# Performance work log

Hardware: AMD Instinct MI355X
Metric: run time of the kernel (lower is better)

The kernel has to match this reference:

```python
import jax, jax.numpy as jnp
import numpy as np

BS = 512          # number of nodes (batch)
EMBED = 256       # embed_dim
NHEAD = 8
HDIM = EMBED // NHEAD
E = BS * BS       # fully-connected intra-batch graph


def _xavier(key, shape):
    lim = float(np.sqrt(6.0 / (shape[0] + shape[1])))
    return jax.random.uniform(key, shape, jnp.float32, -lim, lim)


def setup_inputs() -> dict:
    key = jax.random.key(0)
    ks = jax.random.split(key, 6)
    feats = jax.random.normal(ks[0], (BS, EMBED), jnp.float32)
    # edges sorted by destination c, exactly BS edges per destination
    dst = jnp.repeat(jnp.arange(BS), BS)   # c
    src = jnp.tile(jnp.arange(BS), BS)     # r
    edge_index = jnp.stack([src, dst], axis=1).astype(jnp.int32)  # [E, 2], cols (r, c)
    edge_attr = jnp.zeros((E, 1), jnp.float32)  # unused by forward
    return {
        "feats": feats,
        "edge_index": edge_index,
        "edge_attr": edge_attr,
        "Wq": _xavier(ks[1], (EMBED, EMBED)), "bq": jnp.zeros((EMBED,), jnp.float32),
        "Wk": _xavier(ks[2], (EMBED, EMBED)), "bk": jnp.zeros((EMBED,), jnp.float32),
        "Wv": _xavier(ks[3], (EMBED, EMBED)), "bv": jnp.zeros((EMBED,), jnp.float32),
        "Wo": _xavier(ks[4], (EMBED, EMBED)), "bo": jnp.zeros((EMBED,), jnp.float32),
    }


def reference(feats, edge_index, edge_attr, Wq, bq, Wk, bk, Wv, bv, Wo, bo):
    bs = feats.shape[0]
    scale = 1.0 / np.sqrt(HDIM)
    # QKV projections (torch Linear: x @ W.T + b), split heads -> [h, n, d]
    q = (feats @ Wq.T + bq).reshape(bs, NHEAD, HDIM).transpose(1, 0, 2)
    k = (feats @ Wk.T + bk).reshape(bs, NHEAD, HDIM).transpose(1, 0, 2)
    v = (feats @ Wv.T + bv).reshape(bs, NHEAD, HDIM).transpose(1, 0, 2)
    r, c = edge_index[:, 0], edge_index[:, 1]
    qe = q[:, c, :]   # [h, E, d] query of destination node
    ke = k[:, r, :]   # [h, E, d] key of source node
    ve = v[:, r, :]   # [h, E, d] value of source node
    sim = jnp.einsum('hed,hed->eh', qe, ke) * scale   # [E, h]
    # deterministic segment softmax over edges grouped by destination c
    m = jax.ops.segment_max(sim, c, num_segments=bs)  # [n, h]
    p = jnp.exp(sim - m[c])
    s = jax.ops.segment_sum(p, c, num_segments=bs)    # [n, h]
    attn = p / s[c]                                    # [E, h]
    # weight values and scatter-add per destination (aggr='add')
    out_e = attn.T[..., None] * ve                     # [h, E, d]
    out_e = out_e.transpose(1, 0, 2).reshape(-1, NHEAD * HDIM)  # [E, h*d]
    agg = jax.ops.segment_sum(out_e, c, num_segments=bs)        # [n, embed]
    return agg @ Wo.T + bo
```

## Files before the change

kernel.cpp:

```cpp
#include <hip/hip_runtime.h>

#define BS 512
#define EMBED 256
#define NHEAD 8
#define HDIM 32

typedef __attribute__((ext_vector_type(8))) short short8;
typedef __attribute__((ext_vector_type(4))) float f32x4;

__device__ inline f32x4 mfma16(short8 a, short8 b, f32x4 c) {
    return __builtin_amdgcn_mfma_f32_16x16x32_bf16(a, b, c, 0, 0, 0);
}

__device__ inline unsigned short f2bf(float x) {
    unsigned int u = __float_as_uint(x);
    u += 0x7FFFu + ((u >> 16) & 1u);
    return (unsigned short)(u >> 16);
}
__device__ inline short8 cvt8(const float* p) {
    float4 a = *(const float4*)p;
    float4 b = *(const float4*)(p + 4);
    float x[8] = {a.x, a.y, a.z, a.w, b.x, b.y, b.z, b.w};
    short8 hi;
#pragma unroll
    for (int j = 0; j < 8; ++j) hi[j] = (short)f2bf(x[j]);
    return hi;
}

__global__ __launch_bounds__(256) void qkv_fused(
    const float* __restrict__ feats,
    const float* __restrict__ Wq, const float* __restrict__ Wk,
    const float* __restrict__ Wv, const float* __restrict__ Wo,
    const float* __restrict__ bq, const float* __restrict__ bk,
    const float* __restrict__ bv,
    unsigned short* __restrict__ Qh, unsigned short* __restrict__ Kh,
    unsigned short* __restrict__ Vth, unsigned short* __restrict__ Woh,
    float* __restrict__ OUT)
{
    const int gidx = blockIdx.x * 256 + threadIdx.x;

    if (gidx < 32768) {
        float4 z = {0.f, 0.f, 0.f, 0.f};
        ((float4*)OUT)[gidx] = z;
    }
    if (gidx < 16384) {
        float4 v = ((const float4*)Wo)[gidx];
        const int jrow = gidx >> 6;
        const int c4 = (gidx & 63) * 4;
        const int head = c4 >> 5, dim = c4 & 31;
        const int dst = head * (EMBED * HDIM) + jrow * HDIM + dim;
        ushort4 ph;
        ph.x = f2bf(v.x); ph.y = f2bf(v.y);
        ph.z = f2bf(v.z); ph.w = f2bf(v.w);
        *(ushort4*)(Woh + dst) = ph;
    }

    const int wave = blockIdx.x * 4 + (threadIdx.x >> 6);
    const int l = threadIdx.x & 63;
    const int r = l & 15, g = l >> 4;
    const int nt = wave % 48, mt = wave / 48;
    const int m0 = mt * 16, n0 = nt * 16;
    const int seg = n0 >> 8;
    const int nn = n0 & 255;
    const float* W = (seg == 0) ? Wq : (seg == 1) ? Wk : Wv;
    const float* bias = (seg == 0) ? bq : (seg == 1) ? bk : bv;

    const float* arow = feats + (m0 + r) * EMBED;
    const float* brow = W + (nn + r) * EMBED;

    f32x4 acc = {0.f, 0.f, 0.f, 0.f};
#pragma unroll
    for (int kb = 0; kb < 8; ++kb) {
        const int k0 = kb * 32 + g * 8;
        short8 A = cvt8(arow + k0);
        short8 B = cvt8(brow + k0);
        acc = mfma16(A, B, acc);
    }
    const float bb = bias[nn + r];

    if (seg < 2) {
        unsigned short* D = seg ? Kh : Qh;
        const int cn = nn + r;
        const int head = cn >> 5, dim = cn & 31;
#pragma unroll
        for (int r4 = 0; r4 < 4; ++r4) {
            const int i = m0 + g * 4 + r4;
            D[head * (BS * HDIM) + i * HDIM + dim] = f2bf(acc[r4] + bb);
        }
    } else {
        const int cn = nn + r;
        const int i0 = m0 + g * 4;
        ushort4 ph;
        ph.x = f2bf(acc[0] + bb); ph.y = f2bf(acc[1] + bb);
        ph.z = f2bf(acc[2] + bb); ph.w = f2bf(acc[3] + bb);
        *(ushort4*)(Vth + cn * BS + i0) = ph;
    }
}

__global__ __launch_bounds__(512) void attn_out(
    const unsigned short* __restrict__ Qh, const unsigned short* __restrict__ Kh,
    const unsigned short* __restrict__ Vth, const unsigned short* __restrict__ Woh,
    const float* __restrict__ bo, float* __restrict__ OUT)
{
    const int qt = blockIdx.x >> 3;
    const int h = blockIdx.x & 7;
    const int q0 = qt * 16;
    const int tid = threadIdx.x;
    const int w = tid >> 6, l = tid & 63;
    const int r = l & 15, g = l >> 4;

    __shared__ unsigned short Psm[16 * 512];
    __shared__ float Opart[8][2][256];
    __shared__ float Rpart[8][16];
    __shared__ float Agg[16][36];
    char* Pb = (char*)Psm;

    const short8 qh = *(const short8*)(Qh + h * (BS * HDIM) + (q0 + r) * HDIM + g * 8);
    const unsigned short* Kp = Kh + h * (BS * HDIM);
    short8 kf0 = *(const short8*)(Kp + (w * 64 +  0 + r) * HDIM + g * 8);
    short8 kf1 = *(const short8*)(Kp + (w * 64 + 16 + r) * HDIM + g * 8);
    short8 kf2 = *(const short8*)(Kp + (w * 64 + 32 + r) * HDIM + g * 8);
    short8 kf3 = *(const short8*)(Kp + (w * 64 + 48 + r) * HDIM + g * 8);
    const unsigned short* V0 = Vth + (h * HDIM + r) * BS;
    const unsigned short* V1 = V0 + 16 * BS;
    short8 vf0[2], vf1[2];
#pragma unroll
    for (int kc = 0; kc < 2; ++kc) {
        const int kb = w * 64 + kc * 32 + g * 8;
        vf0[kc] = *(const short8*)(V0 + kb);
        vf1[kc] = *(const short8*)(V1 + kb);
    }
    const unsigned short* Wop = Woh + h * (EMBED * HDIM);
    const short8 bh0 = *(const short8*)(Wop + (w * 32 + r) * HDIM + g * 8);
    const short8 bh1 = *(const short8*)(Wop + (w * 32 + 16 + r) * HDIM + g * 8);

    const float cs = 0.17677669529663687f;
    float rs[4] = {0.f, 0.f, 0.f, 0.f};

#pragma unroll
    for (int kt = 0; kt < 4; ++kt) {
        const short8 kf = (kt == 0) ? kf0 : (kt == 1) ? kf1 : (kt == 2) ? kf2 : kf3;
        const int krow = w * 64 + kt * 16 + r;
        f32x4 acc = {0.f, 0.f, 0.f, 0.f};
        acc = mfma16(qh, kf, acc);
#pragma unroll
        for (int r4 = 0; r4 < 4; ++r4) {
            float p = __expf(acc[r4] * cs);
            rs[r4] += p;
            const int q = g * 4 + r4;
            const int bofs = q * 1024 + ((krow * 2) ^ ((q & 7) << 4));
            *(unsigned short*)(Pb + bofs) = f2bf(p);
        }
    }
#pragma unroll
    for (int off = 1; off < 16; off <<= 1) {
#pragma unroll
        for (int r4 = 0; r4 < 4; ++r4) rs[r4] += __shfl_xor(rs[r4], off);
    }
    if (r == 0) {
#pragma unroll
        for (int r4 = 0; r4 < 4; ++r4) Rpart[w][g * 4 + r4] = rs[r4];
    }

    f32x4 o0 = {0.f, 0.f, 0.f, 0.f}, o1 = {0.f, 0.f, 0.f, 0.f};
#pragma unroll
    for (int kc = 0; kc < 2; ++kc) {
        const int kk = w * 64 + kc * 32 + g * 8;
        const int bofs = r * 1024 + ((kk * 2) ^ ((r & 7) << 4));
        short8 pa = *(const short8*)(Pb + bofs);
        o0 = mfma16(pa, vf0[kc], o0);
        o1 = mfma16(pa, vf1[kc], o1);
    }
    ((f32x4*)&Opart[w][0][0])[l] = o0;
    ((f32x4*)&Opart[w][1][0])[l] = o1;
    __syncthreads();

    if (w < 2) {
        f32x4 o = ((f32x4*)&Opart[0][w][0])[l];
#pragma unroll
        for (int p = 1; p < 8; ++p) {
            f32x4 t = ((f32x4*)&Opart[p][w][0])[l];
            o[0] += t[0]; o[1] += t[1]; o[2] += t[2]; o[3] += t[3];
        }
#pragma unroll
        for (int r4 = 0; r4 < 4; ++r4) {
            const int q = g * 4 + r4;
            float rt = Rpart[0][q];
#pragma unroll
            for (int p = 1; p < 8; ++p) rt += Rpart[p][q];
            Agg[q][w * 16 + r] = o[r4] / rt;
        }
    }
    __syncthreads();

    short8 ah = cvt8(&Agg[r][g * 8]);
    f32x4 a0 = {0.f, 0.f, 0.f, 0.f}, a1 = {0.f, 0.f, 0.f, 0.f};
    a0 = mfma16(ah, bh0, a0);
    a1 = mfma16(ah, bh1, a1);
#pragma unroll
    for (int nsub = 0; nsub < 2; ++nsub) {
        const f32x4 a = nsub ? a1 : a0;
        const int j0 = w * 32 + nsub * 16;
#pragma unroll
        for (int r4 = 0; r4 < 4; ++r4) {
            const int row = q0 + g * 4 + r4;
            const int col = j0 + r;
            float v = a[r4];
            if (h == 0) v += bo[col];
            atomicAdd(&OUT[row * EMBED + col], v);
        }
    }
}

extern "C" void kernel_launch(void* const* d_in, const int* in_sizes, int n_in,
                              void* d_out, int out_size, void* d_ws, size_t ws_size,
                              hipStream_t stream) {
    const float* feats = (const float*)d_in[0];
    const float* Wq = (const float*)d_in[3];
    const float* bq = (const float*)d_in[4];
    const float* Wk = (const float*)d_in[5];
    const float* bk = (const float*)d_in[6];
    const float* Wv = (const float*)d_in[7];
    const float* bv = (const float*)d_in[8];
    const float* Wo = (const float*)d_in[9];
    const float* bo = (const float*)d_in[10];
    float* out = (float*)d_out;

    unsigned short* ws = (unsigned short*)d_ws;
    const size_t NE = (size_t)BS * EMBED;
    unsigned short* Qh  = ws;
    unsigned short* Kh  = Qh + NE;
    unsigned short* Vth = Kh + NE;
    unsigned short* Woh = Vth + NE;

    qkv_fused<<<384, 256, 0, stream>>>(feats, Wq, Wk, Wv, Wo, bq, bk, bv,
                                       Qh, Kh, Vth, Woh, out);
    attn_out<<<256, 512, 0, stream>>>(Qh, Kh, Vth, Woh, bo, out);
}
```

Before: 22.34 us.

## Repartition attention blocks to 8 queries by 2 heads, initialize output with bias

Each attention block now handles 8 query rows for a pair of heads instead of 16 rows for one head. Each wave covers one head and a 128-key segment, and the output projection contracts over 64 dims with a head-pair-packed Wo layout. This halves the number of atomicAdds to the output, since each block now adds two heads at once. The bias is written during the output zero-init rather than added atomically. The cost is that half of each MFMA's rows are duplicated and wasted, because only 8 query rows are used in the 16-row tile.

```diff
diff --git a/kernel.cpp b/kernel.cpp
--- a/kernel.cpp
+++ b/kernel.cpp
@@ -32,7 +32,7 @@
     const float* __restrict__ Wq, const float* __restrict__ Wk,
     const float* __restrict__ Wv, const float* __restrict__ Wo,
     const float* __restrict__ bq, const float* __restrict__ bk,
-    const float* __restrict__ bv,
+    const float* __restrict__ bv, const float* __restrict__ bo,
     unsigned short* __restrict__ Qh, unsigned short* __restrict__ Kh,
     unsigned short* __restrict__ Vth, unsigned short* __restrict__ Woh,
     float* __restrict__ OUT)
@@ -40,15 +40,15 @@
     const int gidx = blockIdx.x * 256 + threadIdx.x;
 
     if (gidx < 32768) {
-        float4 z = {0.f, 0.f, 0.f, 0.f};
-        ((float4*)OUT)[gidx] = z;
+        ((float4*)OUT)[gidx] = ((const float4*)bo)[gidx & 63];
     }
     if (gidx < 16384) {
         float4 v = ((const float4*)Wo)[gidx];
         const int jrow = gidx >> 6;
         const int c4 = (gidx & 63) * 4;
         const int head = c4 >> 5, dim = c4 & 31;
-        const int dst = head * (EMBED * HDIM) + jrow * HDIM + dim;
+        const int dst = (head >> 1) * (EMBED * 2 * HDIM) + jrow * (2 * HDIM)
+                      + (head & 1) * HDIM + dim;
         ushort4 ph;
         ph.x = f2bf(v.x); ph.y = f2bf(v.y);
         ph.z = f2bf(v.z); ph.w = f2bf(v.w);
@@ -100,55 +100,63 @@
 __global__ __launch_bounds__(512) void attn_out(
     const unsigned short* __restrict__ Qh, const unsigned short* __restrict__ Kh,
     const unsigned short* __restrict__ Vth, const unsigned short* __restrict__ Woh,
-    const float* __restrict__ bo, float* __restrict__ OUT)
+    float* __restrict__ OUT)
 {
-    const int qt = blockIdx.x >> 3;
-    const int h = blockIdx.x & 7;
-    const int q0 = qt * 16;
+    const int qt8 = blockIdx.x >> 2;
+    const int hp = blockIdx.x & 3;
+    const int q0 = qt8 * 8;
     const int tid = threadIdx.x;
     const int w = tid >> 6, l = tid & 63;
     const int r = l & 15, g = l >> 4;
-
-    __shared__ unsigned short Psm[16 * 512];
+    const int hh = w & 1;
+    const int head = hp * 2 + hh;
+    const int kseg = w >> 1;
+
+    __shared__ unsigned short Psm[8][8 * 128];
     __shared__ float Opart[8][2][256];
-    __shared__ float Rpart[8][16];
-    __shared__ float Agg[16][36];
-    char* Pb = (char*)Psm;
-
-    const short8 qh = *(const short8*)(Qh + h * (BS * HDIM) + (q0 + r) * HDIM + g * 8);
-    const unsigned short* Kp = Kh + h * (BS * HDIM);
-    short8 kf0 = *(const short8*)(Kp + (w * 64 +  0 + r) * HDIM + g * 8);
-    short8 kf1 = *(const short8*)(Kp + (w * 64 + 16 + r) * HDIM + g * 8);
-    short8 kf2 = *(const short8*)(Kp + (w * 64 + 32 + r) * HDIM + g * 8);
-    short8 kf3 = *(const short8*)(Kp + (w * 64 + 48 + r) * HDIM + g * 8);
-    const unsigned short* V0 = Vth + (h * HDIM + r) * BS;
-    const unsigned short* V1 = V0 + 16 * BS;
-    short8 vf0[2], vf1[2];
-#pragma unroll
-    for (int kc = 0; kc < 2; ++kc) {
-        const int kb = w * 64 + kc * 32 + g * 8;
-        vf0[kc] = *(const short8*)(V0 + kb);
-        vf1[kc] = *(const short8*)(V1 + kb);
-    }
-    const unsigned short* Wop = Woh + h * (EMBED * HDIM);
-    const short8 bh0 = *(const short8*)(Wop + (w * 32 + r) * HDIM + g * 8);
-    const short8 bh1 = *(const short8*)(Wop + (w * 32 + 16 + r) * HDIM + g * 8);
+    __shared__ float Rpart[8][8];
+    __shared__ float Agg[8][68];
+    char* Pb = (char*)&Psm[w][0];
+
+    const short8 qh = *(const short8*)(Qh + head * (BS * HDIM)
+                                       + (q0 + (r & 7)) * HDIM + g * 8);
+    const unsigned short* Kp = Kh + head * (BS * HDIM);
+    short8 kf[8];
+#pragma unroll
+    for (int kt = 0; kt < 8; ++kt) {
+        kf[kt] = *(const short8*)(Kp + (kseg * 128 + kt * 16 + r) * HDIM + g * 8);
+    }
+    short8 vf[2][4];
+#pragma unroll
+    for (int t = 0; t < 2; ++t) {
+#pragma unroll
+        for (int kc = 0; kc < 4; ++kc) {
+            vf[t][kc] = *(const short8*)(Vth + (head * HDIM + t * 16 + r) * BS
+                                         + kseg * 128 + kc * 32 + g * 8);
+        }
+    }
+    const unsigned short* Wop = Woh + hp * (EMBED * 2 * HDIM);
+    short8 bh0[2], bh1[2];
+#pragma unroll
+    for (int ks = 0; ks < 2; ++ks) {
+        bh0[ks] = *(const short8*)(Wop + (w * 32 + r) * 64 + ks * 32 + g * 8);
+        bh1[ks] = *(const short8*)(Wop + (w * 32 + 16 + r) * 64 + ks * 32 + g * 8);
+    }
 
     const float cs = 0.17677669529663687f;
     float rs[4] = {0.f, 0.f, 0.f, 0.f};
 
 #pragma unroll
-    for (int kt = 0; kt < 4; ++kt) {
-        const short8 kf = (kt == 0) ? kf0 : (kt == 1) ? kf1 : (kt == 2) ? kf2 : kf3;
-        const int krow = w * 64 + kt * 16 + r;
+    for (int kt = 0; kt < 8; ++kt) {
+        const int klocal = kt * 16 + r;
         f32x4 acc = {0.f, 0.f, 0.f, 0.f};
-        acc = mfma16(qh, kf, acc);
+        acc = mfma16(qh, kf[kt], acc);
 #pragma unroll
         for (int r4 = 0; r4 < 4; ++r4) {
             float p = __expf(acc[r4] * cs);
             rs[r4] += p;
-            const int q = g * 4 + r4;
-            const int bofs = q * 1024 + ((krow * 2) ^ ((q & 7) << 4));
+            const int q = (g * 4 + r4) & 7;
+            const int bofs = q * 256 + ((klocal * 2) ^ (q << 4));
             *(unsigned short*)(Pb + bofs) = f2bf(p);
         }
     }
@@ -157,57 +165,66 @@
 #pragma unroll
         for (int r4 = 0; r4 < 4; ++r4) rs[r4] += __shfl_xor(rs[r4], off);
     }
-    if (r == 0) {
+    if (r == 0 && g < 2) {
 #pragma unroll
         for (int r4 = 0; r4 < 4; ++r4) Rpart[w][g * 4 + r4] = rs[r4];
     }
 
     f32x4 o0 = {0.f, 0.f, 0.f, 0.f}, o1 = {0.f, 0.f, 0.f, 0.f};
 #pragma unroll
-    for (int kc = 0; kc < 2; ++kc) {
-        const int kk = w * 64 + kc * 32 + g * 8;
-        const int bofs = r * 1024 + ((kk * 2) ^ ((r & 7) << 4));
+    for (int kc = 0; kc < 4; ++kc) {
+        const int kk = kc * 32 + g * 8;
+        const int q = r & 7;
+        const int bofs = q * 256 + ((kk * 2) ^ (q << 4));
         short8 pa = *(const short8*)(Pb + bofs);
-        o0 = mfma16(pa, vf0[kc], o0);
-        o1 = mfma16(pa, vf1[kc], o1);
+        o0 = mfma16(pa, vf[0][kc], o0);
+        o1 = mfma16(pa, vf[1][kc], o1);
     }
     ((f32x4*)&Opart[w][0][0])[l] = o0;
     ((f32x4*)&Opart[w][1][0])[l] = o1;
     __syncthreads();
 
     if (w < 2) {
-        f32x4 o = ((f32x4*)&Opart[0][w][0])[l];
-#pragma unroll
-        for (int p = 1; p < 8; ++p) {
-            f32x4 t = ((f32x4*)&Opart[p][w][0])[l];
-            o[0] += t[0]; o[1] += t[1]; o[2] += t[2]; o[3] += t[3];
-        }
-#pragma unroll
-        for (int r4 = 0; r4 < 4; ++r4) {
-            const int q = g * 4 + r4;
-            float rt = Rpart[0][q];
-#pragma unroll
-            for (int p = 1; p < 8; ++p) rt += Rpart[p][q];
-            Agg[q][w * 16 + r] = o[r4] / rt;
+#pragma unroll
+        for (int t = 0; t < 2; ++t) {
+            f32x4 o = ((f32x4*)&Opart[w][t][0])[l];
+#pragma unroll
+            for (int p = 1; p < 4; ++p) {
+                f32x4 u = ((f32x4*)&Opart[w + 2 * p][t][0])[l];
+                o[0] += u[0]; o[1] += u[1]; o[2] += u[2]; o[3] += u[3];
+            }
+            if (g < 2) {
+#pragma unroll
+                for (int r4 = 0; r4 < 4; ++r4) {
+                    const int q = g * 4 + r4;
+                    const float rt = Rpart[w][q] + Rpart[w + 2][q]
+                                   + Rpart[w + 4][q] + Rpart[w + 6][q];
+                    Agg[q][w * 32 + t * 16 + r] = o[r4] / rt;
+                }
+            }
         }
     }
     __syncthreads();
 
-    short8 ah = cvt8(&Agg[r][g * 8]);
+    short8 ah[2];
+#pragma unroll
+    for (int ks = 0; ks < 2; ++ks) ah[ks] = cvt8(&Agg[r & 7][ks * 32 + g * 8]);
     f32x4 a0 = {0.f, 0.f, 0.f, 0.f}, a1 = {0.f, 0.f, 0.f, 0.f};
-    a0 = mfma16(ah, bh0, a0);
-    a1 = mfma16(ah, bh1, a1);
-#pragma unroll
-    for (int nsub = 0; nsub < 2; ++nsub) {
-        const f32x4 a = nsub ? a1 : a0;
-        const int j0 = w * 32 + nsub * 16;
-#pragma unroll
-        for (int r4 = 0; r4 < 4; ++r4) {
-            const int row = q0 + g * 4 + r4;
-            const int col = j0 + r;
-            float v = a[r4];
-            if (h == 0) v += bo[col];
-            atomicAdd(&OUT[row * EMBED + col], v);
+#pragma unroll
+    for (int ks = 0; ks < 2; ++ks) {
+        a0 = mfma16(ah[ks], bh0[ks], a0);
+        a1 = mfma16(ah[ks], bh1[ks], a1);
+    }
+    if (g < 2) {
+#pragma unroll
+        for (int nsub = 0; nsub < 2; ++nsub) {
+            const f32x4 a = nsub ? a1 : a0;
+            const int j0 = w * 32 + nsub * 16;
+#pragma unroll
+            for (int r4 = 0; r4 < 4; ++r4) {
+                const int row = q0 + g * 4 + r4;
+                atomicAdd(&OUT[row * EMBED + j0 + r], a[r4]);
+            }
         }
     }
 }
@@ -233,7 +250,7 @@
     unsigned short* Vth = Kh + NE;
     unsigned short* Woh = Vth + NE;
 
-    qkv_fused<<<384, 256, 0, stream>>>(feats, Wq, Wk, Wv, Wo, bq, bk, bv,
+    qkv_fused<<<384, 256, 0, stream>>>(feats, Wq, Wk, Wv, Wo, bq, bk, bv, bo,
                                        Qh, Kh, Vth, Woh, out);
-    attn_out<<<256, 512, 0, stream>>>(Qh, Kh, Vth, Woh, bo, out);
-}
+    attn_out<<<256, 512, 0, stream>>>(Qh, Kh, Vth, Woh, out);
+}
```

After: 21.07 us. -5.7%, faster.
